# Kernel tuning notes

Hardware: AMD Instinct MI355X
Metric: run time of the kernel (lower is better)

Reference implementation:

```python
import jax, jax.numpy as jnp
import numpy as np

NUM_QUBITS = 4
NUM_LAYERS = 4
NUM_FILTERS = 4
HIDDEN_DIM = 64
BATCH = 4096
BN_EPS = 1e-5

# ---- batched 4-qubit state-vector gates ----
# state shape: (F_or_1, N, 2, 2, 2, 2); wire w lives on axis 2 + w.

def _rx(state, theta, axis):
    a0 = jnp.take(state, 0, axis=axis)
    a1 = jnp.take(state, 1, axis=axis)
    c = jnp.cos(theta * 0.5).astype(state.dtype)
    s = jnp.sin(theta * 0.5).astype(state.dtype)
    return jnp.stack([c * a0 - 1j * s * a1, -1j * s * a0 + c * a1], axis=axis)

def _rz(state, theta, axis):
    a0 = jnp.take(state, 0, axis=axis)
    a1 = jnp.take(state, 1, axis=axis)
    ph = jnp.exp((-0.5j) * theta.astype(state.dtype))  # e^{-i theta/2}
    return jnp.stack([ph * a0, jnp.conj(ph) * a1], axis=axis)

def _cnot(state, ctrl_axis, tgt_axis):
    # all CNOTs here have tgt_axis < ctrl_axis, so tgt axis index is unchanged
    c0 = jnp.take(state, 0, axis=ctrl_axis)
    c1 = jnp.flip(jnp.take(state, 1, axis=ctrl_axis), axis=tgt_axis)
    return jnp.stack([c0, c1], axis=ctrl_axis)

def _quantum_features(x, qweights):
    # x: (B, 4, 16) -> angles (N=B*16, 4)
    B = x.shape[0]
    F = qweights.shape[0]
    angles = (x * jnp.pi).transpose(0, 2, 1).reshape(-1, NUM_QUBITS)
    half = angles * 0.5
    c, s = jnp.cos(half), jnp.sin(half)
    # RX(angle)|0> = [cos(a/2), -i sin(a/2)] per qubit; build initial state by outer product
    q = jnp.stack([c, -1j * s], axis=-1).astype(jnp.complex64)  # (N, 4, 2)
    state = jnp.einsum('na,nb,nc,nd->nabcd', q[:, 0], q[:, 1], q[:, 2], q[:, 3])[None]  # (1,N,2,2,2,2)
    for layer in range(NUM_LAYERS):
        for i in range(NUM_QUBITS):
            state = _rx(state, qweights[:, layer, i].reshape(F, 1, 1, 1, 1), 2 + i)
        for i in range(NUM_QUBITS):
            state = _rz(state, qweights[:, layer, 4 + i].reshape(F, 1, 1, 1, 1), 2 + i)
        for (cw, tw) in ((3, 2), (2, 1), (1, 0)):
            state = _cnot(state, 2 + cw, 2 + tw)
    probs = jnp.real(state * jnp.conj(state)).astype(jnp.float32)  # (F, N, 2,2,2,2)
    z0 = probs[:, :, 0].sum(axis=(2, 3, 4)) - probs[:, :, 1].sum(axis=(2, 3, 4))  # <Z_0>, (F, N)
    # (F, B, 16) -> (B, F, 16) -> (B, F*16): matches torch stack(dim=1).reshape
    return z0.reshape(F, B, 16).transpose(1, 0, 2).reshape(B, F * 16)


def setup_inputs() -> dict:
    key = jax.random.key(0)
    ks = jax.random.split(key, 8)
    F = NUM_FILTERS
    x = jax.random.uniform(ks[0], (BATCH, NUM_QUBITS, 16), dtype=jnp.float32)
    qweights = 0.05 * jax.random.normal(ks[1], (F, NUM_LAYERS, 8), dtype=jnp.float32)
    fan1 = F * 16
    fc1_w = jax.random.uniform(ks[2], (HIDDEN_DIM, fan1), jnp.float32, -1, 1) / np.sqrt(fan1)
    fc1_b = jax.random.uniform(ks[3], (HIDDEN_DIM,), jnp.float32, -1, 1) / np.sqrt(fan1)
    bn_gamma = jnp.ones((HIDDEN_DIM,), jnp.float32)
    bn_beta = jnp.zeros((HIDDEN_DIM,), jnp.float32)
    fc2_w = jax.random.uniform(ks[4], (1, HIDDEN_DIM), jnp.float32, -1, 1) / np.sqrt(HIDDEN_DIM)
    fc2_b = jax.random.uniform(ks[5], (1,), jnp.float32, -1, 1) / np.sqrt(HIDDEN_DIM)
    return {"x": x, "qweights": qweights, "fc1_w": fc1_w, "fc1_b": fc1_b,
            "bn_gamma": bn_gamma, "bn_beta": bn_beta, "fc2_w": fc2_w, "fc2_b": fc2_b}


def reference(x, qweights, fc1_w, fc1_b, bn_gamma, bn_beta, fc2_w, fc2_b):
    feats = _quantum_features(x, qweights)          # (B, 64)
    h = feats @ fc1_w.T + fc1_b
    h = jax.nn.relu(h)
    mean = h.mean(axis=0)
    var = ((h - mean) ** 2).mean(axis=0)            # biased var (BatchNorm1d, training mode)
    h = (h - mean) / jnp.sqrt(var + BN_EPS) * bn_gamma + bn_beta
    logits = h @ fc2_w.T + fc2_b                    # (B, 1)
    return logits
```

## Files before the change

### kernel.cpp

```cpp
#include <hip/hip_runtime.h>
#include <math.h>

#define BATCH 4096
#define HD 64
static constexpr float BN_EPS = 1e-5f;

__global__ __launch_bounds__(256) void kA(const float* __restrict__ x,
                                          const float* __restrict__ qw,
                                          const float* __restrict__ w1,
                                          const float* __restrict__ b1,
                                          float* __restrict__ h) {
  __shared__ float qc[128];
  __shared__ float qs[128];
  __shared__ float sfeat[4 * 64];

  const int tid = threadIdx.x;
  if (tid < 128) {
    float th = 0.5f * qw[tid];
    __sincosf(th, &qs[tid], &qc[tid]);
  }
  __syncthreads();

  const int bl = tid >> 6;
  const int j = tid & 63;
  const int f = j >> 4;
  const int p = j & 15;
  const int b = blockIdx.x * 4 + bl;

  float cq[4], sq[4];
#pragma unroll
  for (int q = 0; q < 4; ++q) {
    float a = x[b * 64 + q * 16 + p] * (0.5f * (float)M_PI);
    __sincosf(a, &sq[q], &cq[q]);
  }

  float re[16], im[16];
#pragma unroll
  for (int idx = 0; idx < 16; ++idx) {
    float m = 1.f;
#pragma unroll
    for (int q = 0; q < 4; ++q) m *= ((idx >> (3 - q)) & 1) ? sq[q] : cq[q];
    int k = __popc(idx) & 3;
    re[idx] = (k == 0) ? m : ((k == 2) ? -m : 0.f);
    im[idx] = (k == 1) ? -m : ((k == 3) ? m : 0.f);
  }

  const float* qcf = &qc[f * 32];
  const float* qsf = &qs[f * 32];

#pragma unroll
  for (int l = 0; l < 4; ++l) {
#pragma unroll
    for (int w = 0; w < 4; ++w) {
      const float c = qcf[l * 8 + w], s = qsf[l * 8 + w];
      const int mask = 8 >> w;
#pragma unroll
      for (int i0 = 0; i0 < 16; ++i0) {
        if (!(i0 & mask)) {
          const int i1 = i0 | mask;
          float r0 = re[i0], m0 = im[i0], r1 = re[i1], m1 = im[i1];
          re[i0] = c * r0 + s * m1;
          im[i0] = c * m0 - s * r1;
          re[i1] = s * m0 + c * r1;
          im[i1] = -s * r0 + c * m1;
        }
      }
    }
#pragma unroll
    for (int w = 0; w < 4; ++w) {
      const float c = qcf[l * 8 + 4 + w], s = qsf[l * 8 + 4 + w];
      const int mask = 8 >> w;
#pragma unroll
      for (int i = 0; i < 16; ++i) {
        const float sg = (i & mask) ? s : -s;
        float r = re[i], mm = im[i];
        re[i] = c * r - sg * mm;
        im[i] = c * mm + sg * r;
      }
    }
#pragma unroll
    for (int cp = 0; cp < 3; ++cp) {
      const int cmask = 1 << cp;
      const int tmask = 2 << cp;
#pragma unroll
      for (int i = 0; i < 16; ++i) {
        if ((i & cmask) && !(i & tmask)) {
          const int i2 = i | tmask;
          float tr = re[i]; re[i] = re[i2]; re[i2] = tr;
          float ti = im[i]; im[i] = im[i2]; im[i2] = ti;
        }
      }
    }
  }

  float z = 0.f;
#pragma unroll
  for (int i = 0; i < 16; ++i) {
    float pr = re[i] * re[i] + im[i] * im[i];
    z += (i & 8) ? -pr : pr;
  }
  sfeat[bl * 64 + j] = z;
  __syncthreads();

  float acc = b1[j];
  const float* wrow = &w1[j * 64];
  const float* frow = &sfeat[bl * 64];
#pragma unroll
  for (int k = 0; k < 64; ++k) acc = fmaf(frow[k], wrow[k], acc);
  h[b * 64 + j] = fmaxf(acc, 0.f);
}

__global__ __launch_bounds__(256) void kB(const float* __restrict__ h,
                                          const float* __restrict__ gamma,
                                          const float* __restrict__ beta,
                                          float* __restrict__ scale,
                                          float* __restrict__ shift) {
  const int j = blockIdx.x;
  const int tid = threadIdx.x;
  float s = 0.f, s2 = 0.f;
  for (int r = tid; r < BATCH; r += 256) {
    float v = h[r * 64 + j];
    s += v;
    s2 += v * v;
  }
#pragma unroll
  for (int off = 32; off > 0; off >>= 1) {
    s += __shfl_down(s, off, 64);
    s2 += __shfl_down(s2, off, 64);
  }
  __shared__ float ls[4], ls2[4];
  const int wave = tid >> 6, lane = tid & 63;
  if (lane == 0) { ls[wave] = s; ls2[wave] = s2; }
  __syncthreads();
  if (tid == 0) {
    float S = ls[0] + ls[1] + ls[2] + ls[3];
    float S2 = ls2[0] + ls2[1] + ls2[2] + ls2[3];
    float mean = S * (1.f / BATCH);
    float var = S2 * (1.f / BATCH) - mean * mean;
    float sc = gamma[j] / sqrtf(var + BN_EPS);
    scale[j] = sc;
    shift[j] = beta[j] - mean * sc;
  }
}

__global__ __launch_bounds__(256) void kC(const float* __restrict__ h,
                                          const float* __restrict__ scale,
                                          const float* __restrict__ shift,
                                          const float* __restrict__ w2,
                                          const float* __restrict__ b2,
                                          float* __restrict__ out) {
  const int gid = blockIdx.x * 256 + threadIdx.x;
  const int row = gid >> 6;
  const int lane = gid & 63;
  float v = h[row * 64 + lane];
  float t = w2[lane] * (v * scale[lane] + shift[lane]);
#pragma unroll
  for (int off = 32; off > 0; off >>= 1) t += __shfl_down(t, off, 64);
  if (lane == 0) out[row] = t + b2[0];
}

extern "C" void kernel_launch(void* const* d_in, const int* in_sizes, int n_in,
                              void* d_out, int out_size, void* d_ws,
                              size_t ws_size, hipStream_t stream) {
  const float* x = (const float*)d_in[0];
  const float* qw = (const float*)d_in[1];
  const float* w1 = (const float*)d_in[2];
  const float* b1 = (const float*)d_in[3];
  const float* gam = (const float*)d_in[4];
  const float* bet = (const float*)d_in[5];
  const float* w2 = (const float*)d_in[6];
  const float* b2 = (const float*)d_in[7];
  float* out = (float*)d_out;

  float* h = (float*)d_ws;
  float* scale = h + BATCH * 64;
  float* shift = scale + 64;

  kA<<<BATCH / 4, 256, 0, stream>>>(x, qw, w1, b1, h);
  kB<<<64, 256, 0, stream>>>(h, gam, bet, scale, shift);
  kC<<<BATCH / 4, 256, 0, stream>>>(h, scale, shift, w2, b2, out);
}
```

Before: 92.21 us.

## Fuse BN statistics into first kernel via bucketed atomics and simplify gates

Batch-norm sums are now accumulated in the first kernel through bucketed atomicAdds, so the column-strided statistics kernel goes away and only two launches plus a memset remain. The first layer's RX gates are folded into the initial product-state angles, and the four RZ gates per layer are collapsed into one diagonal phase table precomputed in shared memory. w1 is transposed into padded shared memory to avoid strided global reads, and the BN scale and shift are folded into w2. The cost is extra shared memory per block, atomic contention on 32 buckets, and recomputing the statistics reduction in every block of the second kernel.

```diff
diff --git a/kernel.cpp b/kernel.cpp
--- a/kernel.cpp
+++ b/kernel.cpp
@@ -2,24 +2,47 @@
 #include <math.h>
 
 #define BATCH 4096
-#define HD 64
 static constexpr float BN_EPS = 1e-5f;
 
-__global__ __launch_bounds__(256) void kA(const float* __restrict__ x,
+#define GSUM_OFF (BATCH * 64)
+#define GSUM2_OFF (BATCH * 64 + 32 * 64)
+
+__global__ __launch_bounds__(256) void k1(const float* __restrict__ x,
                                           const float* __restrict__ qw,
                                           const float* __restrict__ w1,
                                           const float* __restrict__ b1,
-                                          float* __restrict__ h) {
-  __shared__ float qc[128];
-  __shared__ float qs[128];
-  __shared__ float sfeat[4 * 64];
+                                          float* __restrict__ ws) {
+  __shared__ float qraw[128];
+  __shared__ float qc[128], qs[128];
+  __shared__ float czt[256], szt[256];
+  __shared__ float w1T[65 * 64];
+  __shared__ float hbuf[256];
 
   const int tid = threadIdx.x;
+  if (tid < 128) qraw[tid] = qw[tid];
+  __syncthreads();
+
   if (tid < 128) {
-    float th = 0.5f * qw[tid];
+    float th = 0.5f * qraw[tid];
     __sincosf(th, &qs[tid], &qc[tid]);
   }
-  __syncthreads();
+  {
+    const int f = tid >> 6, l = (tid >> 4) & 3, i = tid & 15;
+    float A = 0.f;
+#pragma unroll
+    for (int w = 0; w < 4; ++w) {
+      float th = qraw[f * 32 + l * 8 + 4 + w];
+      A += ((i >> (3 - w)) & 1) ? th : -th;
+    }
+    A *= 0.5f;
+    __sincosf(A, &szt[tid], &czt[tid]);
+  }
+#pragma unroll
+  for (int m = 0; m < 16; ++m) {
+    int e = tid + 256 * m;
+    int j = e >> 6, k = e & 63;
+    w1T[k * 65 + j] = w1[e];
+  }
 
   const int bl = tid >> 6;
   const int j = tid & 63;
@@ -30,10 +53,9 @@
   float cq[4], sq[4];
 #pragma unroll
   for (int q = 0; q < 4; ++q) {
-    float a = x[b * 64 + q * 16 + p] * (0.5f * (float)M_PI);
+    float a = x[b * 64 + q * 16 + p] * 1.57079632679f + 0.5f * qraw[f * 32 + q];
     __sincosf(a, &sq[q], &cq[q]);
   }
-
   float re[16], im[16];
 #pragma unroll
   for (int idx = 0; idx < 16; ++idx) {
@@ -44,44 +66,43 @@
     re[idx] = (k == 0) ? m : ((k == 2) ? -m : 0.f);
     im[idx] = (k == 1) ? -m : ((k == 3) ? m : 0.f);
   }
+  __syncthreads();
 
   const float* qcf = &qc[f * 32];
   const float* qsf = &qs[f * 32];
+  const float* czf = &czt[f * 64];
+  const float* szf = &szt[f * 64];
 
 #pragma unroll
   for (int l = 0; l < 4; ++l) {
-#pragma unroll
-    for (int w = 0; w < 4; ++w) {
-      const float c = qcf[l * 8 + w], s = qsf[l * 8 + w];
-      const int mask = 8 >> w;
-#pragma unroll
-      for (int i0 = 0; i0 < 16; ++i0) {
-        if (!(i0 & mask)) {
-          const int i1 = i0 | mask;
-          float r0 = re[i0], m0 = im[i0], r1 = re[i1], m1 = im[i1];
-          re[i0] = c * r0 + s * m1;
-          im[i0] = c * m0 - s * r1;
-          re[i1] = s * m0 + c * r1;
-          im[i1] = -s * r0 + c * m1;
+    if (l > 0) {
+#pragma unroll
+      for (int w = 0; w < 4; ++w) {
+        const float c = qcf[l * 8 + w], s = qsf[l * 8 + w];
+        const int mask = 8 >> w;
+#pragma unroll
+        for (int i0 = 0; i0 < 16; ++i0) {
+          if (!(i0 & mask)) {
+            const int i1 = i0 | mask;
+            float r0 = re[i0], m0 = im[i0], r1 = re[i1], m1 = im[i1];
+            re[i0] = c * r0 + s * m1;
+            im[i0] = c * m0 - s * r1;
+            re[i1] = s * m0 + c * r1;
+            im[i1] = -s * r0 + c * m1;
+          }
         }
       }
     }
 #pragma unroll
-    for (int w = 0; w < 4; ++w) {
-      const float c = qcf[l * 8 + 4 + w], s = qsf[l * 8 + 4 + w];
-      const int mask = 8 >> w;
-#pragma unroll
-      for (int i = 0; i < 16; ++i) {
-        const float sg = (i & mask) ? s : -s;
-        float r = re[i], mm = im[i];
-        re[i] = c * r - sg * mm;
-        im[i] = c * mm + sg * r;
-      }
+    for (int i = 0; i < 16; ++i) {
+      const float ca = czf[l * 16 + i], sa = szf[l * 16 + i];
+      float r = re[i], mm = im[i];
+      re[i] = ca * r - sa * mm;
+      im[i] = ca * mm + sa * r;
     }
 #pragma unroll
     for (int cp = 0; cp < 3; ++cp) {
-      const int cmask = 1 << cp;
-      const int tmask = 2 << cp;
+      const int cmask = 1 << cp, tmask = 2 << cp;
 #pragma unroll
       for (int i = 0; i < 16; ++i) {
         if ((i & cmask) && !(i & tmask)) {
@@ -99,61 +120,61 @@
     float pr = re[i] * re[i] + im[i] * im[i];
     z += (i & 8) ? -pr : pr;
   }
-  sfeat[bl * 64 + j] = z;
+  hbuf[bl * 64 + j] = z;
   __syncthreads();
 
   float acc = b1[j];
-  const float* wrow = &w1[j * 64];
-  const float* frow = &sfeat[bl * 64];
-#pragma unroll
-  for (int k = 0; k < 64; ++k) acc = fmaf(frow[k], wrow[k], acc);
-  h[b * 64 + j] = fmaxf(acc, 0.f);
+  const float* frow = &hbuf[bl * 64];
+#pragma unroll
+  for (int k = 0; k < 64; ++k) acc = fmaf(frow[k], w1T[k * 65 + j], acc);
+  const float hval = fmaxf(acc, 0.f);
+  ws[b * 64 + j] = hval;
+
+  __syncthreads();
+  hbuf[bl * 64 + j] = hval;
+  __syncthreads();
+  if (tid < 64) {
+    float s = 0.f, s2 = 0.f;
+#pragma unroll
+    for (int m = 0; m < 4; ++m) {
+      float v = hbuf[m * 64 + tid];
+      s += v;
+      s2 += v * v;
+    }
+    const int bkt = blockIdx.x & 31;
+    atomicAdd(&ws[GSUM_OFF + bkt * 64 + tid], s);
+    atomicAdd(&ws[GSUM2_OFF + bkt * 64 + tid], s2);
+  }
 }
 
-__global__ __launch_bounds__(256) void kB(const float* __restrict__ h,
+__global__ __launch_bounds__(256) void k2(const float* __restrict__ ws,
                                           const float* __restrict__ gamma,
                                           const float* __restrict__ beta,
-                                          float* __restrict__ scale,
-                                          float* __restrict__ shift) {
-  const int j = blockIdx.x;
-  const int tid = threadIdx.x;
-  float s = 0.f, s2 = 0.f;
-  for (int r = tid; r < BATCH; r += 256) {
-    float v = h[r * 64 + j];
-    s += v;
-    s2 += v * v;
-  }
-#pragma unroll
-  for (int off = 32; off > 0; off >>= 1) {
-    s += __shfl_down(s, off, 64);
-    s2 += __shfl_down(s2, off, 64);
-  }
-  __shared__ float ls[4], ls2[4];
-  const int wave = tid >> 6, lane = tid & 63;
-  if (lane == 0) { ls[wave] = s; ls2[wave] = s2; }
-  __syncthreads();
-  if (tid == 0) {
-    float S = ls[0] + ls[1] + ls[2] + ls[3];
-    float S2 = ls2[0] + ls2[1] + ls2[2] + ls2[3];
-    float mean = S * (1.f / BATCH);
-    float var = S2 * (1.f / BATCH) - mean * mean;
-    float sc = gamma[j] / sqrtf(var + BN_EPS);
-    scale[j] = sc;
-    shift[j] = beta[j] - mean * sc;
-  }
-}
-
-__global__ __launch_bounds__(256) void kC(const float* __restrict__ h,
-                                          const float* __restrict__ scale,
-                                          const float* __restrict__ shift,
                                           const float* __restrict__ w2,
                                           const float* __restrict__ b2,
                                           float* __restrict__ out) {
-  const int gid = blockIdx.x * 256 + threadIdx.x;
-  const int row = gid >> 6;
-  const int lane = gid & 63;
-  float v = h[row * 64 + lane];
-  float t = w2[lane] * (v * scale[lane] + shift[lane]);
+  __shared__ float wsc[64], wsh[64];
+  const int tid = threadIdx.x;
+  if (tid < 64) {
+    float s = 0.f, s2 = 0.f;
+#pragma unroll
+    for (int k = 0; k < 32; ++k) {
+      s += ws[GSUM_OFF + k * 64 + tid];
+      s2 += ws[GSUM2_OFF + k * 64 + tid];
+    }
+    float mean = s * (1.f / BATCH);
+    float var = s2 * (1.f / BATCH) - mean * mean;
+    float sc = gamma[tid] / sqrtf(var + BN_EPS);
+    float sh = beta[tid] - mean * sc;
+    float w = w2[tid];
+    wsc[tid] = w * sc;
+    wsh[tid] = w * sh;
+  }
+  __syncthreads();
+
+  const int row = blockIdx.x * 4 + (tid >> 6);
+  const int lane = tid & 63;
+  float t = fmaf(ws[row * 64 + lane], wsc[lane], wsh[lane]);
 #pragma unroll
   for (int off = 32; off > 0; off >>= 1) t += __shfl_down(t, off, 64);
   if (lane == 0) out[row] = t + b2[0];
@@ -171,12 +192,9 @@
   const float* w2 = (const float*)d_in[6];
   const float* b2 = (const float*)d_in[7];
   float* out = (float*)d_out;
-
-  float* h = (float*)d_ws;
-  float* scale = h + BATCH * 64;
-  float* shift = scale + 64;
-
-  kA<<<BATCH / 4, 256, 0, stream>>>(x, qw, w1, b1, h);
-  kB<<<64, 256, 0, stream>>>(h, gam, bet, scale, shift);
-  kC<<<BATCH / 4, 256, 0, stream>>>(h, scale, shift, w2, b2, out);
+  float* ws = (float*)d_ws;
+
+  hipMemsetAsync(ws + GSUM_OFF, 0, 2 * 32 * 64 * sizeof(float), stream);
+  k1<<<BATCH / 4, 256, 0, stream>>>(x, qw, w1, b1, ws);
+  k2<<<BATCH / 4, 256, 0, stream>>>(ws, gam, bet, w2, b2, out);
 }
```

Measured after the change: 79.95 us. 13.3% less time.
